# Kernel optimization log

Hardware: AMD Instinct MI355X
Metric: run time of the kernel (lower is better)

The kernel has to match this reference:

```python
import jax, jax.numpy as jnp
import numpy as np

DELTA1 = 0.025
EXP_INT = 1          # exponent_interfaces
L_SING = 2.0 / 3.0   # singular exponent l returned by explain heads
R0 = 0.5             # radius of the radial cutoff rc
EPS = 1e-12
S1, S2, S3, S4 = 1.0, 2.0, 3.0, 4.0
N = 1 << 20          # n/4 points per interface segment
HID = 64


def lelu(x):
    return jnp.abs(x)


def relcut_C0(x):
    return jax.nn.relu(x) - jax.nn.relu(x - 1.0)


def bc_cutoff(x, y):
    return (1.0 - x * x) * (1.0 - y * y)


def explain(xy, W1, b1, W2, b2):
    # NN head: [n,2] -> (p1, px, py), plus analytic rc, l, r
    h = jnp.tanh(xy @ W1 + b1)            # [n, HID]
    out = h @ W2 + b2                     # [n, 3]
    p1, px, py = out[:, 0], out[:, 1], out[:, 2]
    r = jnp.sqrt(jnp.sum(xy * xy, axis=-1) + EPS)
    rc = jnp.maximum(1.0 - r / R0, 0.0) ** 2
    return p1, px, py, rc, L_SING, r


def _full_jump_x(sp, jp, sleft, sright, u, sign):
    y0 = u * sign
    x0z = jnp.zeros_like(y0)

    def phi_sum(x0):
        xy = jnp.stack([x0, y0], axis=-1)
        bc = bc_cutoff(x0, y0)
        jp1, jpx, jpy, _, _, _ = explain(xy, *jp)
        sp1, spx, spy, rc, l, r = explain(xy, *sp)
        smooth_sing = (sp1 + spy * lelu(y0 / r)) * rc * r ** l
        smooth_jump = bc * (jp1 + jpy * lelu(y0))
        return jnp.sum(smooth_sing + smooth_jump)

    dphi1 = jax.grad(phi_sum)(x0z)        # d phi / d x at x=0, elementwise
    xy0 = jnp.stack([x0z, y0], axis=-1)
    bc = bc_cutoff(x0z, y0)
    _, jpx, _, _, _, _ = explain(xy0, *jp)
    _, spx, _, rc, l, r = explain(xy0, *sp)
    sing_fact = rc * r ** (l - 1.0)
    corr = jpx * bc + spx * sing_fact
    dleft = dphi1 - corr
    dright = dphi1 + corr
    omega = relcut_C0(jnp.abs(y0 / DELTA1)) ** EXP_INT
    return jnp.mean((sleft * dleft - sright * dright) ** 2 * omega)


def _full_jump_y(sp, jp, stop, sbottom, u, sign):
    x0 = u * sign
    y0z = jnp.zeros_like(x0)

    def phi_sum(y0):
        xy = jnp.stack([x0, y0], axis=-1)
        bc = bc_cutoff(x0, y0)
        jp1, jpx, jpy, _, _, _ = explain(xy, *jp)
        sp1, spx, spy, rc, l, r = explain(xy, *sp)
        smooth_sing = (sp1 + spx * lelu(x0 / r)) * rc * r ** l
        smooth_jump = bc * (jp1 + jpx * lelu(x0))
        return jnp.sum(smooth_sing + smooth_jump)

    dphi1 = jax.grad(phi_sum)(y0z)        # d phi / d y at y=0, elementwise
    xy0 = jnp.stack([x0, y0z], axis=-1)
    bc = bc_cutoff(x0, y0z)
    _, _, jpy, _, _, _ = explain(xy0, *jp)
    _, _, spy, rc, l, r = explain(xy0, *sp)
    sing_fact = rc * r ** (l - 1.0)
    corr = jpy * bc + spy * sing_fact
    dbottom = dphi1 - corr
    dtop = dphi1 + corr
    omega = relcut_C0(jnp.abs(x0 / DELTA1)) ** EXP_INT
    return jnp.mean((sbottom * dbottom - stop * dtop) ** 2 * omega)


def setup_inputs() -> dict:
    key = jax.random.key(0)
    ks = jax.random.split(key, 12)
    f32 = jnp.float32
    return {
        "u_y1": jax.random.uniform(ks[0], (N,), dtype=f32),
        "u_ym1": jax.random.uniform(ks[1], (N,), dtype=f32),
        "u_x1": jax.random.uniform(ks[2], (N,), dtype=f32),
        "u_xm1": jax.random.uniform(ks[3], (N,), dtype=f32),
        "sing_W1": jax.random.normal(ks[4], (2, HID), dtype=f32) * 0.5,
        "sing_b1": jax.random.normal(ks[5], (HID,), dtype=f32) * 0.1,
        "sing_W2": jax.random.normal(ks[6], (HID, 3), dtype=f32) * 0.2,
        "sing_b2": jax.random.normal(ks[7], (3,), dtype=f32) * 0.1,
        "jump_W1": jax.random.normal(ks[8], (2, HID), dtype=f32) * 0.5,
        "jump_b1": jax.random.normal(ks[9], (HID,), dtype=f32) * 0.1,
        "jump_W2": jax.random.normal(ks[10], (HID, 3), dtype=f32) * 0.2,
        "jump_b2": jax.random.normal(ks[11], (3,), dtype=f32) * 0.1,
    }


def reference(u_y1, u_ym1, u_x1, u_xm1,
              sing_W1, sing_b1, sing_W2, sing_b2,
              jump_W1, jump_b1, jump_W2, jump_b2):
    sp = (sing_W1, sing_b1, sing_W2, sing_b2)
    jp = (jump_W1, jump_b1, jump_W2, jump_b2)
    jump_y_1 = _full_jump_y(sp, jp, S1, S4, u_y1, 1.0)
    jump_y_m1 = _full_jump_y(sp, jp, S2, S3, u_ym1, -1.0)
    jump_x_1 = _full_jump_x(sp, jp, S2, S1, u_x1, 1.0)
    jump_x_m1 = _full_jump_x(sp, jp, S3, S4, u_xm1, -1.0)
    return jump_y_1 + jump_y_m1 + jump_x_1 + jump_x_m1
```

## Files before the change

kernel.cpp:

```cpp
#include <hip/hip_runtime.h>

#define NS (1 << 20)
#define THREADS 256
#define TABN 4096

#define MILP 16
#define MSPB (THREADS * MILP)
#define MBPS (NS / MSPB)
#define MGRID (4 * MBPS)

#define BBPS (TABN / THREADS)
#define BGRID (4 * BBPS)

#define FILP 8
#define FSPB (THREADS * FILP)
#define FBPS (NS / FSPB)
#define FGRID (4 * FBPS)

#define WS_NEED ((size_t)(4096 + TABN * 4 * sizeof(float2)))

typedef float v2f __attribute__((ext_vector_type(2)));


__global__ __launch_bounds__(THREADS) void build_tab(
    const float* __restrict__ sW1, const float* __restrict__ sb1,
    const float* __restrict__ sW2, const float* __restrict__ sb2,
    const float* __restrict__ jW1, const float* __restrict__ jb1,
    const float* __restrict__ jW2, const float* __restrict__ jb2,
    float2* __restrict__ tab)
{
    __shared__ __align__(16) float s_w[64][12];
    __shared__ float s_swv[2];

    const int bid = blockIdx.x;
    const int seg = bid / BBPS;
    const int nodeblk = bid - seg * BBPS;
    const int tid = threadIdx.x;

    const int ca  = (seg < 2) ? 0 : 1;
    const int pp  = 1 - ca;
    const int kv  = (seg < 2) ? 2 : 1;
    const int kd2 = 3 - kv;
    const float sign  = (seg & 1) ? -1.0f : 1.0f;
    const float alpha = (seg == 0) ? 3.0f : ((seg == 3) ? -1.0f : 1.0f);
    const float beta  = (seg <  2) ? -5.0f : ((seg == 2) ? -3.0f : -7.0f);

    const float TL = 2.885390081777927f;

    if (tid < 64) {
        const int j = tid;
        float sw1c = sW1[ca * 64 + j], jw1c = jW1[ca * 64 + j];
        float sw1p = sW1[pp * 64 + j], jw1p = jW1[pp * 64 + j];
        s_w[j][0] = sw1c * TL * sign;
        s_w[j][1] = jw1c * TL * sign;
        s_w[j][2] = sb1[j] * TL;
        s_w[j][3] = jb1[j] * TL;
        s_w[j][4] = 4.0f * sw1p * sW2[j * 3 + 0];
        s_w[j][5] = 4.0f * jw1p * jW2[j * 3 + 0];
        s_w[j][6] = 4.0f * sw1p * sW2[j * 3 + kd2];
        s_w[j][7] = 4.0f * jw1p * jW2[j * 3 + kd2];
        s_w[j][8] = sW2[j * 3 + kv];
        s_w[j][9] = jW2[j * 3 + kv];
    }
    __syncthreads();
    if (tid < 2) {
        float s = 0.0f;
        for (int j = 0; j < 64; ++j) s += s_w[j][8 + tid];
        s_swv[tid] = s + (tid ? jb2[kv] : sb2[kv]);
    }
    __syncthreads();

    const int node = nodeblk * THREADS + tid;
    const float uu[2] = {(float)node * (1.0f / TABN),
                         (float)(node + 1) * (1.0f / TABN)};

    float Vgs[2] = {0, 0}, D0s[2] = {0, 0}, D2s[2] = {0, 0};
    float Vgj[2] = {0, 0}, D0j[2] = {0, 0}, D2j[2] = {0, 0};

    for (int j = 0; j < 64; ++j) {
        const float4 A = *(const float4*)&s_w[j][0];
        const float4 B = *(const float4*)&s_w[j][4];
        const v2f   wv = *(const v2f*)&s_w[j][8];
        #pragma unroll
        for (int s = 0; s < 2; ++s) {
            float ps = fmaf(A.x, uu[s], A.z);
            float Es = __builtin_amdgcn_exp2f(ps);
            float gs = __builtin_amdgcn_rcpf(Es + 1.0f);
            float ts = fmaf(-gs, gs, gs);
            Vgs[s] = fmaf(gs, wv.x, Vgs[s]);
            D0s[s] = fmaf(ts, B.x, D0s[s]);
            D2s[s] = fmaf(ts, B.z, D2s[s]);
            float pj = fmaf(A.y, uu[s], A.w);
            float Ej = __builtin_amdgcn_exp2f(pj);
            float gj = __builtin_amdgcn_rcpf(Ej + 1.0f);
            float tj = fmaf(-gj, gj, gj);
            Vgj[s] = fmaf(gj, wv.y, Vgj[s]);
            D0j[s] = fmaf(tj, B.y, D0j[s]);
            D2j[s] = fmaf(tj, B.w, D2j[s]);
        }
    }

    const float swv_s = s_swv[0], swv_j = s_swv[1];
    float G[2];
    #pragma unroll
    for (int s = 0; s < 2; ++s) {
        const float u = uu[s];
        float r = __builtin_amdgcn_sqrtf(fmaf(u, u, 1e-12f));
        float inv_r = __builtin_amdgcn_rcpf(r);
        float rcb = fmaxf(fmaf(-2.0f, r, 1.0f), 0.0f);
        float rc = rcb * rcb;
        float rl = __builtin_amdgcn_exp2f(0.66666666666666663f * __builtin_amdgcn_logf(r));
        float rcrl = rc * rl;
        float rcrlm1 = rcrl * inv_r;
        float q = u * inv_r;
        float bcv = fmaf(-u, u, 1.0f);
        float wgt = fminf(40.0f * u, 1.0f);
        float VS = fmaf(-2.0f, Vgs[s], swv_s);
        float VJ = fmaf(-2.0f, Vgj[s], swv_j);
        float dphi1 = fmaf(D2s[s], q, D0s[s]) * rcrl
                    + bcv * fmaf(D2j[s], u, D0j[s]);
        float corr = VJ * bcv + VS * rcrlm1;
        float val = fmaf(alpha, dphi1, beta * corr);
        G[s] = val * val * wgt;
    }

    tab[seg * TABN + node] = make_float2(G[0], G[1] - G[0]);
}

__global__ __launch_bounds__(THREADS) void eval_main(
    const float* __restrict__ u0p, const float* __restrict__ u1p,
    const float* __restrict__ u2p, const float* __restrict__ u3p,
    const float2* __restrict__ tab, float* __restrict__ partials)
{
    __shared__ __align__(16) float2 s_tab[TABN];
    __shared__ float s_red[THREADS / 64];

    const int bid = blockIdx.x;
    const int seg = bid >> 8;
    const int chunk = bid & 255;
    const int tid = threadIdx.x;

    {
        const float4* src = (const float4*)(tab + seg * TABN);
        float4* dst = (float4*)s_tab;
        #pragma unroll
        for (int t = 0; t < 8; ++t)
            dst[t * THREADS + tid] = src[t * THREADS + tid];
    }
    __syncthreads();

    const float* up = (seg == 0) ? u0p : (seg == 1) ? u1p : (seg == 2) ? u2p : u3p;
    const float4* up4 = (const float4*)up;

    float acc = 0.0f;
    #pragma unroll
    for (int t = 0; t < MILP / 4; ++t) {
        float4 u4 = up4[chunk * (MSPB / 4) + t * THREADS + tid];
        float us[4] = {u4.x, u4.y, u4.z, u4.w};
        #pragma unroll
        for (int s = 0; s < 4; ++s) {
            float fidx = us[s] * (float)TABN;
            int i = (int)fidx;
            i = (i < TABN - 1) ? i : (TABN - 1);
            float f = fidx - (float)i;
            float2 T = s_tab[i];
            acc += fmaf(f, T.y, T.x);
        }
    }

    #pragma unroll
    for (int off = 32; off; off >>= 1) acc += __shfl_down(acc, off);
    const int lane = tid & 63, wid = tid >> 6;
    if (lane == 0) s_red[wid] = acc;
    __syncthreads();
    if (tid == 0) partials[bid] = s_red[0] + s_red[1] + s_red[2] + s_red[3];
}

__global__ __launch_bounds__(256) void jump_loss_stage2(
    const float* __restrict__ partials, float* __restrict__ out, int n)
{
    double s = 0.0;
    for (int i = threadIdx.x; i < n; i += 256) s += (double)partials[i];
    #pragma unroll
    for (int off = 32; off; off >>= 1) s += __shfl_down(s, off);
    __shared__ double sr[4];
    int lane = threadIdx.x & 63, wid = threadIdx.x >> 6;
    if (lane == 0) sr[wid] = s;
    __syncthreads();
    if (threadIdx.x == 0) {
        out[0] = (float)((sr[0] + sr[1] + sr[2] + sr[3]) / (double)NS);
    }
}

__global__ __launch_bounds__(THREADS, 4) void direct_stage1(
    const float* __restrict__ u0p, const float* __restrict__ u1p,
    const float* __restrict__ u2p, const float* __restrict__ u3p,
    const float* __restrict__ sW1, const float* __restrict__ sb1,
    const float* __restrict__ sW2, const float* __restrict__ sb2,
    const float* __restrict__ jW1, const float* __restrict__ jb1,
    const float* __restrict__ jW2, const float* __restrict__ jb2,
    float* __restrict__ out)
{
    __shared__ __align__(16) float s_w[64][12];
    __shared__ float s_swv[2];
    __shared__ float s_red[THREADS / 64];

    const int bid = blockIdx.x;
    const int seg = bid / FBPS;
    const int chunk = bid - seg * FBPS;
    const int tid = threadIdx.x;

    const int ca  = (seg < 2) ? 0 : 1;
    const int pp  = 1 - ca;
    const int kv  = (seg < 2) ? 2 : 1;
    const int kd2 = 3 - kv;
    const float sign  = (seg & 1) ? -1.0f : 1.0f;
    const float alpha = (seg == 0) ? 3.0f : ((seg == 3) ? -1.0f : 1.0f);
    const float beta  = (seg <  2) ? -5.0f : ((seg == 2) ? -3.0f : -7.0f);
    const float TL = 2.885390081777927f;

    if (tid < 64) {
        const int j = tid;
        float sw1c = sW1[ca * 64 + j], jw1c = jW1[ca * 64 + j];
        float sw1p = sW1[pp * 64 + j], jw1p = jW1[pp * 64 + j];
        s_w[j][0] = sw1c * TL * sign;
        s_w[j][1] = jw1c * TL * sign;
        s_w[j][2] = sb1[j] * TL;
        s_w[j][3] = jb1[j] * TL;
        s_w[j][4] = 4.0f * sw1p * sW2[j * 3 + 0];
        s_w[j][5] = 4.0f * jw1p * jW2[j * 3 + 0];
        s_w[j][6] = 4.0f * sw1p * sW2[j * 3 + kd2];
        s_w[j][7] = 4.0f * jw1p * jW2[j * 3 + kd2];
        s_w[j][8] = sW2[j * 3 + kv];
        s_w[j][9] = jW2[j * 3 + kv];
    }
    __syncthreads();
    if (tid < 2) {
        float s = 0.0f;
        for (int j = 0; j < 64; ++j) s += s_w[j][8 + tid];
        s_swv[tid] = s + (tid ? jb2[kv] : sb2[kv]);
    }
    __syncthreads();

    const float* up = (seg == 0) ? u0p : (seg == 1) ? u1p : (seg == 2) ? u2p : u3p;
    const float4* up4 = (const float4*)up;
    const int base = chunk * (FSPB / 4) + tid;
    const float4 a4 = up4[base];
    const float4 b4 = up4[base + THREADS];
    const float uu[FILP] = {a4.x, a4.y, a4.z, a4.w, b4.x, b4.y, b4.z, b4.w};

    float Vgs[FILP], D0s[FILP], D2s[FILP], Vgj[FILP], D0j[FILP], D2j[FILP];
    #pragma unroll
    for (int s = 0; s < FILP; ++s) {
        Vgs[s] = 0.0f; D0s[s] = 0.0f; D2s[s] = 0.0f;
        Vgj[s] = 0.0f; D0j[s] = 0.0f; D2j[s] = 0.0f;
    }

    #pragma unroll 2
    for (int j = 0; j < 64; ++j) {
        const float4 A = *(const float4*)&s_w[j][0];
        const float4 B = *(const float4*)&s_w[j][4];
        const v2f   wv = *(const v2f*)&s_w[j][8];
        #pragma unroll
        for (int s = 0; s < FILP; ++s) {
            float ps = fmaf(A.x, uu[s], A.z);
            float Es = __builtin_amdgcn_exp2f(ps);
            float gs = __builtin_amdgcn_rcpf(Es + 1.0f);
            float ts = fmaf(-gs, gs, gs);
            Vgs[s] = fmaf(gs, wv.x, Vgs[s]);
            D0s[s] = fmaf(ts, B.x, D0s[s]);
            D2s[s] = fmaf(ts, B.z, D2s[s]);
            float pj = fmaf(A.y, uu[s], A.w);
            float Ej = __builtin_amdgcn_exp2f(pj);
            float gj = __builtin_amdgcn_rcpf(Ej + 1.0f);
            float tj = fmaf(-gj, gj, gj);
            Vgj[s] = fmaf(gj, wv.y, Vgj[s]);
            D0j[s] = fmaf(tj, B.y, D0j[s]);
            D2j[s] = fmaf(tj, B.w, D2j[s]);
        }
    }

    const float swv_s = s_swv[0], swv_j = s_swv[1];
    float acc = 0.0f;
    #pragma unroll
    for (int s = 0; s < FILP; ++s) {
        const float u = uu[s];
        float r = __builtin_amdgcn_sqrtf(fmaf(u, u, 1e-12f));
        float inv_r = __builtin_amdgcn_rcpf(r);
        float rcb = fmaxf(fmaf(-2.0f, r, 1.0f), 0.0f);
        float rc = rcb * rcb;
        float rl = __builtin_amdgcn_exp2f(0.66666666666666663f * __builtin_amdgcn_logf(r));
        float rcrl = rc * rl;
        float rcrlm1 = rcrl * inv_r;
        float q = u * inv_r;
        float bcv = fmaf(-u, u, 1.0f);
        float wgt = fminf(40.0f * u, 1.0f);
        float VS = fmaf(-2.0f, Vgs[s], swv_s);
        float VJ = fmaf(-2.0f, Vgj[s], swv_j);
        float dphi1 = fmaf(D2s[s], q, D0s[s]) * rcrl
                    + bcv * fmaf(D2j[s], u, D0j[s]);
        float corr = VJ * bcv + VS * rcrlm1;
        float val = fmaf(alpha, dphi1, beta * corr);
        acc = fmaf(val * val, wgt, acc);
    }

    #pragma unroll
    for (int off = 32; off; off >>= 1) acc += __shfl_down(acc, off);
    const int lane = tid & 63, wid = tid >> 6;
    if (lane == 0) s_red[wid] = acc;
    __syncthreads();
    if (tid == 0) {
        float bs = s_red[0] + s_red[1] + s_red[2] + s_red[3];
        atomicAdd(out, bs * (1.0f / (float)NS));
    }
}

extern "C" void kernel_launch(void* const* d_in, const int* in_sizes, int n_in,
                              void* d_out, int out_size, void* d_ws, size_t ws_size,
                              hipStream_t stream) {
    const float* u_y1  = (const float*)d_in[0];
    const float* u_ym1 = (const float*)d_in[1];
    const float* u_x1  = (const float*)d_in[2];
    const float* u_xm1 = (const float*)d_in[3];
    const float* sW1 = (const float*)d_in[4];
    const float* sb1 = (const float*)d_in[5];
    const float* sW2 = (const float*)d_in[6];
    const float* sb2 = (const float*)d_in[7];
    const float* jW1 = (const float*)d_in[8];
    const float* jb1 = (const float*)d_in[9];
    const float* jW2 = (const float*)d_in[10];
    const float* jb2 = (const float*)d_in[11];
    float* out = (float*)d_out;

    if (ws_size >= WS_NEED) {
        float*  partials = (float*)d_ws;
        float2* tab = (float2*)((char*)d_ws + 4096);
        build_tab<<<BGRID, THREADS, 0, stream>>>(
            sW1, sb1, sW2, sb2, jW1, jb1, jW2, jb2, tab);
        eval_main<<<MGRID, THREADS, 0, stream>>>(
            u_y1, u_ym1, u_x1, u_xm1, tab, partials);
        jump_loss_stage2<<<1, 256, 0, stream>>>(partials, out, MGRID);
    } else {
        hipMemsetAsync(d_out, 0, sizeof(float), stream);
        direct_stage1<<<FGRID, THREADS, 0, stream>>>(
            u_y1, u_ym1, u_x1, u_xm1, sW1, sb1, sW2, sb2, jW1, jb1, jW2, jb2,
            out);
    }
}
```

Baseline: 18.39 us.

## Split table build across lanes, store scalar nodes, fuse final reduction via atomics

The table builder now assigns four threads per node, each summing 16 of the 64 hidden units, and combines them with lane shuffles. Each node is evaluated once and stored as a single float rather than as a (value, delta) pair, which halves the table size. The eval kernel now interpolates from two adjacent entries. The separate final-reduction kernel is removed: each block adds a fixed-point scaled sum into a 64-bit atomic counter, and the last block to finish writes the output. This saves one kernel launch and shortens the serial build, at the cost of fixed-point quantisation and relying on counters reset by the previous kernel.

```diff
diff --git a/kernel.cpp b/kernel.cpp
--- a/kernel.cpp
+++ b/kernel.cpp
@@ -3,21 +3,24 @@
 #define NS (1 << 20)
 #define THREADS 256
 #define TABN 4096
+#define TABSTRIDE 4160
+
+#define BNODES 64
+#define BBPS 65
+#define BGRID (4 * BBPS)
 
 #define MILP 16
 #define MSPB (THREADS * MILP)
 #define MBPS (NS / MSPB)
 #define MGRID (4 * MBPS)
 
-#define BBPS (TABN / THREADS)
-#define BGRID (4 * BBPS)
-
 #define FILP 8
 #define FSPB (THREADS * FILP)
 #define FBPS (NS / FSPB)
 #define FGRID (4 * FBPS)
 
-#define WS_NEED ((size_t)(4096 + TABN * 4 * sizeof(float2)))
+#define SCALE 262144.0
+#define WS_NEED ((size_t)(256 + 4 * TABSTRIDE * sizeof(float)))
 
 typedef float v2f __attribute__((ext_vector_type(2)));
 
@@ -27,15 +30,17 @@
     const float* __restrict__ sW2, const float* __restrict__ sb2,
     const float* __restrict__ jW1, const float* __restrict__ jb1,
     const float* __restrict__ jW2, const float* __restrict__ jb2,
-    float2* __restrict__ tab)
+    float* __restrict__ tab, unsigned long long* __restrict__ ctrs)
 {
     __shared__ __align__(16) float s_w[64][12];
     __shared__ float s_swv[2];
 
     const int bid = blockIdx.x;
     const int seg = bid / BBPS;
-    const int nodeblk = bid - seg * BBPS;
+    const int blk = bid - seg * BBPS;
     const int tid = threadIdx.x;
+
+    if (bid == 0 && tid == 0) { ctrs[0] = 0ull; ctrs[1] = 0ull; }
 
     const int ca  = (seg < 2) ? 0 : 1;
     const int pp  = 1 - ca;
@@ -44,7 +49,6 @@
     const float sign  = (seg & 1) ? -1.0f : 1.0f;
     const float alpha = (seg == 0) ? 3.0f : ((seg == 3) ? -1.0f : 1.0f);
     const float beta  = (seg <  2) ? -5.0f : ((seg == 2) ? -3.0f : -7.0f);
-
     const float TL = 2.885390081777927f;
 
     if (tid < 64) {
@@ -70,69 +74,65 @@
     }
     __syncthreads();
 
-    const int node = nodeblk * THREADS + tid;
-    const float uu[2] = {(float)node * (1.0f / TABN),
-                         (float)(node + 1) * (1.0f / TABN)};
-
-    float Vgs[2] = {0, 0}, D0s[2] = {0, 0}, D2s[2] = {0, 0};
-    float Vgj[2] = {0, 0}, D0j[2] = {0, 0}, D2j[2] = {0, 0};
-
-    for (int j = 0; j < 64; ++j) {
+    const int part = tid & 3;
+    const int node = blk * BNODES + (tid >> 2);
+    const float u = (float)node * (1.0f / TABN);
+
+    float Vgs = 0.0f, D0s = 0.0f, D2s = 0.0f, Vgj = 0.0f, D0j = 0.0f, D2j = 0.0f;
+    #pragma unroll 4
+    for (int jj = 0; jj < 16; ++jj) {
+        const int j = (part << 4) | jj;
         const float4 A = *(const float4*)&s_w[j][0];
         const float4 B = *(const float4*)&s_w[j][4];
         const v2f   wv = *(const v2f*)&s_w[j][8];
-        #pragma unroll
-        for (int s = 0; s < 2; ++s) {
-            float ps = fmaf(A.x, uu[s], A.z);
-            float Es = __builtin_amdgcn_exp2f(ps);
-            float gs = __builtin_amdgcn_rcpf(Es + 1.0f);
-            float ts = fmaf(-gs, gs, gs);
-            Vgs[s] = fmaf(gs, wv.x, Vgs[s]);
-            D0s[s] = fmaf(ts, B.x, D0s[s]);
-            D2s[s] = fmaf(ts, B.z, D2s[s]);
-            float pj = fmaf(A.y, uu[s], A.w);
-            float Ej = __builtin_amdgcn_exp2f(pj);
-            float gj = __builtin_amdgcn_rcpf(Ej + 1.0f);
-            float tj = fmaf(-gj, gj, gj);
-            Vgj[s] = fmaf(gj, wv.y, Vgj[s]);
-            D0j[s] = fmaf(tj, B.y, D0j[s]);
-            D2j[s] = fmaf(tj, B.w, D2j[s]);
-        }
-    }
-
-    const float swv_s = s_swv[0], swv_j = s_swv[1];
-    float G[2];
-    #pragma unroll
-    for (int s = 0; s < 2; ++s) {
-        const float u = uu[s];
-        float r = __builtin_amdgcn_sqrtf(fmaf(u, u, 1e-12f));
-        float inv_r = __builtin_amdgcn_rcpf(r);
-        float rcb = fmaxf(fmaf(-2.0f, r, 1.0f), 0.0f);
-        float rc = rcb * rcb;
-        float rl = __builtin_amdgcn_exp2f(0.66666666666666663f * __builtin_amdgcn_logf(r));
-        float rcrl = rc * rl;
-        float rcrlm1 = rcrl * inv_r;
-        float q = u * inv_r;
-        float bcv = fmaf(-u, u, 1.0f);
-        float wgt = fminf(40.0f * u, 1.0f);
-        float VS = fmaf(-2.0f, Vgs[s], swv_s);
-        float VJ = fmaf(-2.0f, Vgj[s], swv_j);
-        float dphi1 = fmaf(D2s[s], q, D0s[s]) * rcrl
-                    + bcv * fmaf(D2j[s], u, D0j[s]);
-        float corr = VJ * bcv + VS * rcrlm1;
-        float val = fmaf(alpha, dphi1, beta * corr);
-        G[s] = val * val * wgt;
-    }
-
-    tab[seg * TABN + node] = make_float2(G[0], G[1] - G[0]);
+        float ps = fmaf(A.x, u, A.z);
+        float Es = __builtin_amdgcn_exp2f(ps);
+        float gs = __builtin_amdgcn_rcpf(Es + 1.0f);
+        float ts = fmaf(-gs, gs, gs);
+        Vgs = fmaf(gs, wv.x, Vgs);
+        D0s = fmaf(ts, B.x, D0s);
+        D2s = fmaf(ts, B.z, D2s);
+        float pj = fmaf(A.y, u, A.w);
+        float Ej = __builtin_amdgcn_exp2f(pj);
+        float gj = __builtin_amdgcn_rcpf(Ej + 1.0f);
+        float tj = fmaf(-gj, gj, gj);
+        Vgj = fmaf(gj, wv.y, Vgj);
+        D0j = fmaf(tj, B.y, D0j);
+        D2j = fmaf(tj, B.w, D2j);
+    }
+    #pragma unroll
+    for (int m = 1; m <= 2; m <<= 1) {
+        Vgs += __shfl_xor(Vgs, m); D0s += __shfl_xor(D0s, m); D2s += __shfl_xor(D2s, m);
+        Vgj += __shfl_xor(Vgj, m); D0j += __shfl_xor(D0j, m); D2j += __shfl_xor(D2j, m);
+    }
+
+    float r = __builtin_amdgcn_sqrtf(fmaf(u, u, 1e-12f));
+    float inv_r = __builtin_amdgcn_rcpf(r);
+    float rcb = fmaxf(fmaf(-2.0f, r, 1.0f), 0.0f);
+    float rc = rcb * rcb;
+    float rl = __builtin_amdgcn_exp2f(0.66666666666666663f * __builtin_amdgcn_logf(r));
+    float rcrl = rc * rl;
+    float rcrlm1 = rcrl * inv_r;
+    float q = u * inv_r;
+    float bcv = fmaf(-u, u, 1.0f);
+    float wgt = fminf(40.0f * u, 1.0f);
+    float VS = fmaf(-2.0f, Vgs, s_swv[0]);
+    float VJ = fmaf(-2.0f, Vgj, s_swv[1]);
+    float dphi1 = fmaf(D2s, q, D0s) * rcrl + bcv * fmaf(D2j, u, D0j);
+    float corr = VJ * bcv + VS * rcrlm1;
+    float val = fmaf(alpha, dphi1, beta * corr);
+    float G = val * val * wgt;
+
+    if (part == 0 && node <= TABN) tab[seg * TABSTRIDE + node] = G;
 }
 
 __global__ __launch_bounds__(THREADS) void eval_main(
     const float* __restrict__ u0p, const float* __restrict__ u1p,
     const float* __restrict__ u2p, const float* __restrict__ u3p,
-    const float2* __restrict__ tab, float* __restrict__ partials)
+    const float* __restrict__ tab, unsigned long long* __restrict__ ctrs,
+    float* __restrict__ out)
 {
-    __shared__ __align__(16) float2 s_tab[TABN];
+    __shared__ __align__(16) float s_tab[TABN + 4];
     __shared__ float s_red[THREADS / 64];
 
     const int bid = blockIdx.x;
@@ -141,11 +141,12 @@
     const int tid = threadIdx.x;
 
     {
-        const float4* src = (const float4*)(tab + seg * TABN);
+        const float4* src = (const float4*)(tab + seg * TABSTRIDE);
         float4* dst = (float4*)s_tab;
         #pragma unroll
-        for (int t = 0; t < 8; ++t)
+        for (int t = 0; t < 4; ++t)
             dst[t * THREADS + tid] = src[t * THREADS + tid];
+        if (tid == 0) s_tab[TABN] = tab[seg * TABSTRIDE + TABN];
     }
     __syncthreads();
 
@@ -163,8 +164,9 @@
             int i = (int)fidx;
             i = (i < TABN - 1) ? i : (TABN - 1);
             float f = fidx - (float)i;
-            float2 T = s_tab[i];
-            acc += fmaf(f, T.y, T.x);
+            float T0 = s_tab[i];
+            float T1 = s_tab[i + 1];
+            acc += fmaf(f, T1 - T0, T0);
         }
     }
 
@@ -173,22 +175,16 @@
     const int lane = tid & 63, wid = tid >> 6;
     if (lane == 0) s_red[wid] = acc;
     __syncthreads();
-    if (tid == 0) partials[bid] = s_red[0] + s_red[1] + s_red[2] + s_red[3];
-}
-
-__global__ __launch_bounds__(256) void jump_loss_stage2(
-    const float* __restrict__ partials, float* __restrict__ out, int n)
-{
-    double s = 0.0;
-    for (int i = threadIdx.x; i < n; i += 256) s += (double)partials[i];
-    #pragma unroll
-    for (int off = 32; off; off >>= 1) s += __shfl_down(s, off);
-    __shared__ double sr[4];
-    int lane = threadIdx.x & 63, wid = threadIdx.x >> 6;
-    if (lane == 0) sr[wid] = s;
-    __syncthreads();
-    if (threadIdx.x == 0) {
-        out[0] = (float)((sr[0] + sr[1] + sr[2] + sr[3]) / (double)NS);
+    if (tid == 0) {
+        float bs = s_red[0] + s_red[1] + s_red[2] + s_red[3];
+        unsigned long long iv = (unsigned long long)(long long)((double)bs * SCALE);
+        atomicAdd(&ctrs[0], iv);
+        __threadfence();
+        unsigned long long prev = atomicAdd(&ctrs[1], 1ull);
+        if (prev == (unsigned long long)(MGRID - 1)) {
+            unsigned long long tot = atomicAdd(&ctrs[0], 0ull);
+            out[0] = (float)((double)(long long)tot * (1.0 / (SCALE * (double)NS)));
+        }
     }
 }
 
@@ -333,13 +329,12 @@
     float* out = (float*)d_out;
 
     if (ws_size >= WS_NEED) {
-        float*  partials = (float*)d_ws;
-        float2* tab = (float2*)((char*)d_ws + 4096);
+        unsigned long long* ctrs = (unsigned long long*)d_ws;
+        float* tab = (float*)((char*)d_ws + 256);
         build_tab<<<BGRID, THREADS, 0, stream>>>(
-            sW1, sb1, sW2, sb2, jW1, jb1, jW2, jb2, tab);
+            sW1, sb1, sW2, sb2, jW1, jb1, jW2, jb2, tab, ctrs);
         eval_main<<<MGRID, THREADS, 0, stream>>>(
-            u_y1, u_ym1, u_x1, u_xm1, tab, partials);
-        jump_loss_stage2<<<1, 256, 0, stream>>>(partials, out, MGRID);
+            u_y1, u_ym1, u_x1, u_xm1, tab, ctrs, out);
     } else {
         hipMemsetAsync(d_out, 0, sizeof(float), stream);
         direct_stage1<<<FGRID, THREADS, 0, stream>>>(
```

Result: slower. 39.30 us (+113.7%).
